# Performance work log

Measured on AMD Instinct MI355X. Metric: run time of the kernel, lower is better.

The kernel has to match this reference:

```python
import jax, jax.numpy as jnp
import numpy as np

IMG = 224
PATCH = 16
EMBED = 768
C = 12
B = 64

def setup_inputs() -> dict:
    key = jax.random.key(0)
    k1, k2 = jax.random.split(key)
    x = jax.random.normal(k1, (B, C, IMG, IMG), dtype=jnp.float32)
    channel_weights = jax.random.normal(k2, (C, EMBED), dtype=jnp.float32)
    return {"x": x, "channel_weights": channel_weights}

def reference(x, channel_weights):
    # Original torch code builds a [E, C, K, K] conv weight by replicating each
    # channel_weights[c, e] across the full KxK kernel, then does a stride-K conv.
    # That is mathematically a per-patch KxK sum-pool followed by a C->E matmul.
    Bb, Cc, H, W = x.shape
    K = PATCH
    n = H // K  # patches per side (14)
    # [B, C, n, K, n, K] -> sum over kernel dims -> [B, C, n, n]
    pooled = x.reshape(Bb, Cc, n, K, n, K).sum(axis=(3, 5))
    # contract channel dim with [C, E] weights -> [B, n, n, E]
    out = jnp.einsum('bcij,ce->bije', pooled, channel_weights)
    return out.reshape(Bb, n * n, EMBED)
```

## Files before the change

### kernel.cpp

```cpp
#include <hip/hip_runtime.h>


#define BATCH 64
#define CH    12
#define IMGD  224
#define NP    14
#define NPP   (NP * NP)
#define EMB   768
#define E4    (EMB / 4)

typedef float vfloat4 __attribute__((ext_vector_type(4)));

__global__ __launch_bounds__(384) void dcsp_fused_kernel(
    const float* __restrict__ x,
    const float* __restrict__ w,
    float* __restrict__ out)
{
    const int blk = blockIdx.x;
    const int b  = blk / (NP * (NP / 2));
    const int r0 = blk - b * (NP * (NP / 2));
    const int i  = r0 / (NP / 2);
    const int jj = r0 - i * (NP / 2);

    const int t    = threadIdx.x;
    const int lane = t & 63;
    const int wave = t >> 6;

    __shared__ float pooled[2][CH];

    const int r8 = lane >> 3;
    const int q  = lane & 7;
    const int colbase = jj * 32 + q * 4;

    float s[2] = {0.f, 0.f};
#pragma unroll
    for (int k = 0; k < 2; ++k) {
        const int c = wave * 2 + k;
        const size_t chbase = (size_t)(b * CH + c) * IMGD * IMGD;
#pragma unroll
        for (int half = 0; half < 2; ++half) {
            const int row = i * 16 + half * 8 + r8;
            const vfloat4 v = __builtin_nontemporal_load(
                reinterpret_cast<const vfloat4*>(
                    x + chbase + (size_t)row * IMGD + colbase));
            s[k] += (v.x + v.y) + (v.z + v.w);
        }
    }

#pragma unroll
    for (int m = 0; m < 5; ++m) {
        const int mask = (1 << m) < 4 ? (1 << m) : (1 << (m + 1));
#pragma unroll
        for (int k = 0; k < 2; ++k)
            s[k] += __shfl_xor(s[k], mask, 64);
    }
    if (lane == 0) {
        pooled[0][wave * 2 + 0] = s[0];
        pooled[0][wave * 2 + 1] = s[1];
    } else if (lane == 4) {
        pooled[1][wave * 2 + 0] = s[0];
        pooled[1][wave * 2 + 1] = s[1];
    }
    __syncthreads();

    const int patch = t / E4;
    const int e4    = t - patch * E4;

    vfloat4 acc = (vfloat4){0.f, 0.f, 0.f, 0.f};
    const vfloat4* __restrict__ w4 = reinterpret_cast<const vfloat4*>(w);
#pragma unroll
    for (int c = 0; c < CH; ++c) {
        const float   pc = pooled[patch][c];
        const vfloat4 wv = w4[c * E4 + e4];
        acc += pc * wv;
    }
    const int j = jj * 2 + patch;
    vfloat4* o4 = reinterpret_cast<vfloat4*>(out) +
                  (((size_t)(b * NPP) + i * NP + j) * E4 + e4);
    __builtin_nontemporal_store(acc, o4);
}

extern "C" void kernel_launch(void* const* d_in, const int* in_sizes, int n_in,
                              void* d_out, int out_size, void* d_ws, size_t ws_size,
                              hipStream_t stream) {
    const float* x = (const float*)d_in[0];
    const float* w = (const float*)d_in[1];
    float* out = (float*)d_out;

    dcsp_fused_kernel<<<BATCH * NP * (NP / 2), 384, 0, stream>>>(x, w, out);
}
```

Before: 222.1 us.

## Assign one patch-pair task per wave, removing shared memory and block sync

Each wave now handles a whole two-patch task by itself: it loads all 12 channels, reduces them with shuffles and computes the full 768-wide projection for both patches. A block holds four independent waves. This drops the LDS staging and the __syncthreads, and gives each thread more loads in flight. In exchange each thread does more shuffles (12 channels), uses more registers, and issues more weight loads per output.

Result: slower. 236.5 us (+6.5%).

```diff
diff --git a/kernel.cpp b/kernel.cpp
--- a/kernel.cpp
+++ b/kernel.cpp
@@ -11,73 +11,62 @@
 
 typedef float vfloat4 __attribute__((ext_vector_type(4)));
 
-__global__ __launch_bounds__(384) void dcsp_fused_kernel(
+__global__ __launch_bounds__(256) void dcsp_wave_kernel(
     const float* __restrict__ x,
     const float* __restrict__ w,
     float* __restrict__ out)
 {
-    const int blk = blockIdx.x;
-    const int b  = blk / (NP * (NP / 2));
-    const int r0 = blk - b * (NP * (NP / 2));
-    const int i  = r0 / (NP / 2);
-    const int jj = r0 - i * (NP / 2);
-
     const int t    = threadIdx.x;
     const int lane = t & 63;
     const int wave = t >> 6;
 
-    __shared__ float pooled[2][CH];
+    const int task = blockIdx.x * 4 + wave;
+    const int b  = task / (NP * (NP / 2));
+    const int r0 = task - b * (NP * (NP / 2));
+    const int i  = r0 / (NP / 2);
+    const int jj = r0 - i * (NP / 2);
 
     const int r8 = lane >> 3;
     const int q  = lane & 7;
-    const int colbase = jj * 32 + q * 4;
+    const size_t rowoff0 = (size_t)(i * 16 + r8) * IMGD + (jj * 32 + q * 4);
+    const size_t rowoff1 = rowoff0 + (size_t)8 * IMGD;
 
-    float s[2] = {0.f, 0.f};
+    float s[CH];
 #pragma unroll
-    for (int k = 0; k < 2; ++k) {
-        const int c = wave * 2 + k;
-        const size_t chbase = (size_t)(b * CH + c) * IMGD * IMGD;
-#pragma unroll
-        for (int half = 0; half < 2; ++half) {
-            const int row = i * 16 + half * 8 + r8;
-            const vfloat4 v = __builtin_nontemporal_load(
-                reinterpret_cast<const vfloat4*>(
-                    x + chbase + (size_t)row * IMGD + colbase));
-            s[k] += (v.x + v.y) + (v.z + v.w);
-        }
+    for (int c = 0; c < CH; ++c) {
+        const float* __restrict__ base =
+            x + (size_t)(b * CH + c) * (IMGD * IMGD);
+        const vfloat4 a = __builtin_nontemporal_load(
+            reinterpret_cast<const vfloat4*>(base + rowoff0));
+        const vfloat4 d = __builtin_nontemporal_load(
+            reinterpret_cast<const vfloat4*>(base + rowoff1));
+        s[c] = ((a.x + a.y) + (a.z + a.w)) + ((d.x + d.y) + (d.z + d.w));
     }
 
 #pragma unroll
     for (int m = 0; m < 5; ++m) {
         const int mask = (1 << m) < 4 ? (1 << m) : (1 << (m + 1));
 #pragma unroll
-        for (int k = 0; k < 2; ++k)
-            s[k] += __shfl_xor(s[k], mask, 64);
+        for (int c = 0; c < CH; ++c)
+            s[c] += __shfl_xor(s[c], mask, 64);
     }
-    if (lane == 0) {
-        pooled[0][wave * 2 + 0] = s[0];
-        pooled[0][wave * 2 + 1] = s[1];
-    } else if (lane == 4) {
-        pooled[1][wave * 2 + 0] = s[0];
-        pooled[1][wave * 2 + 1] = s[1];
+
+    const int half = q >> 2;
+    const int lidx = r8 * 4 + (q & 3);
+    const int j = jj * 2 + half;
+    const vfloat4* __restrict__ w4 = reinterpret_cast<const vfloat4*>(w);
+    vfloat4* __restrict__ orow = reinterpret_cast<vfloat4*>(out) +
+        ((size_t)(b * NPP) + i * NP + j) * E4;
+
+#pragma unroll
+    for (int k = 0; k < 6; ++k) {
+        const int e4 = lidx + 32 * k;
+        vfloat4 acc = (vfloat4){0.f, 0.f, 0.f, 0.f};
+#pragma unroll
+        for (int c = 0; c < CH; ++c)
+            acc += s[c] * w4[c * E4 + e4];
+        __builtin_nontemporal_store(acc, orow + e4);
     }
-    __syncthreads();
-
-    const int patch = t / E4;
-    const int e4    = t - patch * E4;
-
-    vfloat4 acc = (vfloat4){0.f, 0.f, 0.f, 0.f};
-    const vfloat4* __restrict__ w4 = reinterpret_cast<const vfloat4*>(w);
-#pragma unroll
-    for (int c = 0; c < CH; ++c) {
-        const float   pc = pooled[patch][c];
-        const vfloat4 wv = w4[c * E4 + e4];
-        acc += pc * wv;
-    }
-    const int j = jj * 2 + patch;
-    vfloat4* o4 = reinterpret_cast<vfloat4*>(out) +
-                  (((size_t)(b * NPP) + i * NP + j) * E4 + e4);
-    __builtin_nontemporal_store(acc, o4);
 }
 
 extern "C" void kernel_launch(void* const* d_in, const int* in_sizes, int n_in,
@@ -87,5 +76,5 @@
     const float* w = (const float*)d_in[1];
     float* out = (float*)d_out;
 
-    dcsp_fused_kernel<<<BATCH * NP * (NP / 2), 384, 0, stream>>>(x, w, out);
+    dcsp_wave_kernel<<<BATCH * NP * (NP / 2) / 4, 256, 0, stream>>>(x, w, out);
 }
```
